# Kernel optimization log

Hardware: AMD Instinct MI355X
Metric: run time of the kernel (lower is better)

Reference implementation:

```python
import jax, jax.numpy as jnp
import numpy as np

LAMBDA = 0.95   # fast-weight decay
ETA = 0.5       # Hebbian write rate
EPS = 1e-5      # LayerNorm epsilon
S_LOOP = 2      # inner read steps


def setup_inputs() -> dict:
    key = jax.random.key(0)
    ks = jax.random.split(key, 3)
    T, B, d_g, d_h = 32, 32, 256, 512
    z_seq = jax.random.normal(ks[0], (T, B, d_g), dtype=jnp.float32)
    # kaiming-uniform-ish / xavier-ish scaled weights
    W_h = jax.random.normal(ks[1], (d_h, d_h), dtype=jnp.float32) * (2.0 / d_h) ** 0.5
    W_g = jax.random.normal(ks[2], (d_h, d_g), dtype=jnp.float32) * (2.0 / (d_h + d_g)) ** 0.5
    b_h = jnp.zeros((d_h,), jnp.float32)
    ln_gamma = jnp.ones((d_h,), jnp.float32)
    ln_beta = jnp.zeros((d_h,), jnp.float32)
    return {"z_seq": z_seq, "W_h": W_h, "W_g": W_g, "b_h": b_h,
            "ln_gamma": ln_gamma, "ln_beta": ln_beta}


def reference(z_seq, W_h, W_g, b_h, ln_gamma, ln_beta):
    T, B, _ = z_seq.shape
    d_h = W_h.shape[0]

    def ln(x):
        mu = jnp.mean(x, axis=-1, keepdims=True)
        var = jnp.mean((x - mu) ** 2, axis=-1, keepdims=True)
        return (x - mu) * jax.lax.rsqrt(var + EPS) * ln_gamma + ln_beta

    def inner_read(h_base, A):
        # h = relu(LN(h_base)); then S fast-weight reads h <- relu(LN(h_base + A h))
        h = jax.nn.relu(ln(h_base))
        for _ in range(S_LOOP):
            Ah = jnp.einsum('bij,bj->bi', A, h)  # [B, d_h]
            h = jax.nn.relu(ln(h_base + Ah))
        return h

    def step(carry, z_t):
        h, A = carry
        h_base = h @ W_h.T + z_t @ W_g.T + b_h  # [B, d_h]
        h = inner_read(h_base, A)
        # Hebbian outer-product write: A <- lambda*A + eta * h h^T
        A = LAMBDA * A + ETA * jnp.einsum('bi,bj->bij', h, h)
        return (h, A), None

    h0 = jnp.zeros((B, d_h), z_seq.dtype)
    A0 = jnp.zeros((B, d_h, d_h), z_seq.dtype)
    (h, A), _ = jax.lax.scan(step, (h0, A0), z_seq[:-1])

    # last step: read-only (no A update)
    h_base = h @ W_h.T + z_seq[-1] @ W_g.T + b_h
    h = inner_read(h_base, A)
    return h
```

## Files before the change

### kernel.cpp

```cpp
#include <hip/hip_runtime.h>

constexpr int T_STEPS = 32;
constexpr int BATCH   = 32;
constexpr int DG      = 256;
constexpr int DH      = 512;
constexpr int NHIST   = 31;
constexpr float LAMBDA_ = 0.95f;
constexpr float ETA_    = 0.5f;
constexpr float EPS_    = 1e-5f;

__global__ __launch_bounds__(512) void aux_kernel(
    const float* __restrict__ z, const float* __restrict__ Wg,
    const float* __restrict__ bh, float* __restrict__ ZG,
    const float* __restrict__ Wh, uint4* __restrict__ Wp) {
  const int tid = threadIdx.x;
  if (blockIdx.x < 256) {
    const int lane = tid & 63;
    const int wave = tid >> 6;
    const int tb0  = blockIdx.x * 4;
    float4 zv[4];
#pragma unroll
    for (int p = 0; p < 4; ++p)
      zv[p] = *reinterpret_cast<const float4*>(z + (size_t)(tb0 + p) * DG + lane * 4);
    for (int k = 0; k < 64; ++k) {
      const int r = wave * 64 + k;
      const float4 wv = *reinterpret_cast<const float4*>(Wg + (size_t)r * DG + lane * 4);
      float a0 = zv[0].x*wv.x + zv[0].y*wv.y + zv[0].z*wv.z + zv[0].w*wv.w;
      float a1 = zv[1].x*wv.x + zv[1].y*wv.y + zv[1].z*wv.z + zv[1].w*wv.w;
      float a2 = zv[2].x*wv.x + zv[2].y*wv.y + zv[2].z*wv.z + zv[2].w*wv.w;
      float a3 = zv[3].x*wv.x + zv[3].y*wv.y + zv[3].z*wv.z + zv[3].w*wv.w;
#pragma unroll
      for (int off = 32; off; off >>= 1) {
        a0 += __shfl_xor(a0, off, 64);
        a1 += __shfl_xor(a1, off, 64);
        a2 += __shfl_xor(a2, off, 64);
        a3 += __shfl_xor(a3, off, 64);
      }
      if (lane == 0) {
        const float bb = bh[r];
        ZG[(size_t)(tb0 + 0) * DH + r] = a0 + bb;
        ZG[(size_t)(tb0 + 1) * DH + r] = a1 + bb;
        ZG[(size_t)(tb0 + 2) * DH + r] = a2 + bb;
        ZG[(size_t)(tb0 + 3) * DH + r] = a3 + bb;
      }
    }
  } else {
    const int v = (blockIdx.x - 256) * 512 + tid;
    const int r = v >> 6;
    const int k8h = v & 63;
    const float4 a = *reinterpret_cast<const float4*>(Wh + (size_t)r * DH + k8h * 8);
    const float4 b = *reinterpret_cast<const float4*>(Wh + (size_t)r * DH + k8h * 8 + 4);
    auto cvt = [](float f) -> uint {
      uint u = __float_as_uint(f);
      return (u + 0x7FFFu + ((u >> 16) & 1u)) >> 16;
    };
    uint4 o;
    o.x = cvt(a.x) | (cvt(a.y) << 16);
    o.y = cvt(a.z) | (cvt(a.w) << 16);
    o.z = cvt(b.x) | (cvt(b.y) << 16);
    o.w = cvt(b.z) | (cvt(b.w) << 16);
    Wp[(size_t)k8h * DH + r] = o;
  }
}

__global__ __launch_bounds__(1024) void rnn_kernel(
    const uint4* __restrict__ Wp, const float* __restrict__ ZG,
    const float* __restrict__ g, const float* __restrict__ be,
    float* __restrict__ out) {
  __shared__ alignas(16) float hist[40][DH];
  __shared__ alignas(16) float4 h4_s[DH / 4];
  __shared__ float part[DH];
  __shared__ float cc[NHIST];
  __shared__ float red1[16], red2[16];
  __shared__ float lam_pow[NHIST];

  float* h_s = reinterpret_cast<float*>(h4_s);
  const int tid  = threadIdx.x;
  const int lane = tid & 63;
  const int wave = tid >> 6;
  const int r    = tid & 511;
  const int kh   = tid >> 9;
  const int b    = blockIdx.x;
  const bool own = (kh == 0);

  if (tid == 0) {
    float p = 1.f;
    for (int k = 0; k < NHIST; ++k) { lam_pow[k] = p; p *= LAMBDA_; }
  }
  float g_r = 0.f, be_r = 0.f;
  if (own) { g_r = g[r]; be_r = be[r]; }

  auto ln = [&](float x) -> float {
    float s1 = own ? x : 0.f;
    float s2 = own ? x * x : 0.f;
#pragma unroll
    for (int off = 32; off; off >>= 1) {
      s1 += __shfl_xor(s1, off, 64);
      s2 += __shfl_xor(s2, off, 64);
    }
    if (lane == 0) { red1[wave] = s1; red2[wave] = s2; }
    __syncthreads();
    float a = 0.f, q = 0.f;
#pragma unroll
    for (int w2 = 0; w2 < 16; ++w2) { a += red1[w2]; q += red2[w2]; }
    const float mu = a * (1.f / DH);
    const float rs = rsqrtf(q * (1.f / DH) - mu * mu + EPS_);
    float hv = 0.f;
    if (own) {
      hv = fmaxf((x - mu) * rs * g_r + be_r, 0.f);
      h_s[r] = hv;
    }
    __syncthreads();
    return hv;
  };

  float hv = 0.f;
  for (int t = 0; t < T_STEPS; ++t) {
    const float* zg = ZG + ((size_t)t * BATCH + b) * DH;
    float xb;

    if (t == 0) {
      xb = own ? zg[r] : 0.f;
    } else {
      const uint4* wp = Wp + (size_t)(kh * 32) * DH + r;
      const float4* hh = h4_s + kh * 64;
      float acc = 0.f;
#pragma unroll 4
      for (int k8 = 0; k8 < 32; ++k8) {
        const uint4 wv = wp[(size_t)k8 * DH];
        const float4 ha = hh[k8 * 2];
        const float4 hb = hh[k8 * 2 + 1];
        acc = fmaf(__uint_as_float(wv.x << 16),           ha.x, acc);
        acc = fmaf(__uint_as_float(wv.x & 0xFFFF0000u),   ha.y, acc);
        acc = fmaf(__uint_as_float(wv.y << 16),           ha.z, acc);
        acc = fmaf(__uint_as_float(wv.y & 0xFFFF0000u),   ha.w, acc);
        acc = fmaf(__uint_as_float(wv.z << 16),           hb.x, acc);
        acc = fmaf(__uint_as_float(wv.z & 0xFFFF0000u),   hb.y, acc);
        acc = fmaf(__uint_as_float(wv.w << 16),           hb.z, acc);
        acc = fmaf(__uint_as_float(wv.w & 0xFFFF0000u),   hb.w, acc);
      }
      if (!own) part[r] = acc;
      __syncthreads();
      xb = own ? (acc + part[r] + zg[r]) : 0.f;
    }

    hv = ln(xb);

    if (t > 0) {
      for (int s = 0; s < 2; ++s) {
        const float4 c0 = *reinterpret_cast<const float4*>(h_s + lane * 8);
        const float4 c1 = *reinterpret_cast<const float4*>(h_s + lane * 8 + 4);
        for (int sp = wave; sp < t; sp += 16) {
          const float* hr = hist[sp];
          const float4 a0 = *reinterpret_cast<const float4*>(hr + lane * 8);
          const float4 a1 = *reinterpret_cast<const float4*>(hr + lane * 8 + 4);
          float d = c0.x*a0.x + c0.y*a0.y + c0.z*a0.z + c0.w*a0.w
                  + c1.x*a1.x + c1.y*a1.y + c1.z*a1.z + c1.w*a1.w;
#pragma unroll
          for (int off = 32; off; off >>= 1) d += __shfl_xor(d, off, 64);
          if (lane == 0) cc[sp] = ETA_ * lam_pow[t - 1 - sp] * d;
        }
        __syncthreads();
        float x2 = xb;
        if (own) {
          float ah = 0.f;
          for (int sp = 0; sp < t; ++sp) ah = fmaf(cc[sp], hist[sp][r], ah);
          x2 = xb + ah;
        }
        hv = ln(x2);
      }
    }

    if (own && t < T_STEPS - 1) hist[t][r] = hv;
  }

  if (own) out[(size_t)b * DH + r] = hv;
}

extern "C" void kernel_launch(void* const* d_in, const int* in_sizes, int n_in,
                              void* d_out, int out_size, void* d_ws, size_t ws_size,
                              hipStream_t stream) {
  const float* z     = (const float*)d_in[0];
  const float* W_h   = (const float*)d_in[1];
  const float* W_g   = (const float*)d_in[2];
  const float* b_h   = (const float*)d_in[3];
  const float* gamma = (const float*)d_in[4];
  const float* beta  = (const float*)d_in[5];
  float* out = (float*)d_out;

  float* ZG = (float*)d_ws;
  uint4* Wp = (uint4*)((char*)d_ws + (size_t)T_STEPS * BATCH * DH * 4);

  aux_kernel<<<dim3(320), dim3(512), 0, stream>>>(z, W_g, b_h, ZG, W_h, Wp);
  rnn_kernel<<<dim3(BATCH), dim3(1024), 0, stream>>>(Wp, ZG, gamma, beta, out);
}
```

Baseline: 340.4 us.

## Use bf16 MFMA for recurrent matvec and pack two batch rows per block

Rewrites the per-step W_h·h product as 16x16x32 bf16 MFMA tiles, with W_h pre-packed into an MFMA-friendly tile layout and h stored as bf16 in shared memory. Each block now processes two batch rows, which halves the grid to 16 blocks and puts all 1024 threads to use instead of half of them being idle during LayerNorm. Half of each wave's weight fragments are prefetched into registers across time steps. The cost is that h is now rounded to bf16 before the matvec, only 2 of 16 MFMA columns do useful work, and fewer CUs are busy.

```diff
diff --git a/kernel.cpp b/kernel.cpp
--- a/kernel.cpp
+++ b/kernel.cpp
@@ -1,13 +1,22 @@
 #include <hip/hip_runtime.h>
+
+typedef __attribute__((ext_vector_type(8))) short short8;
+typedef __attribute__((ext_vector_type(4))) float f32x4;
 
 constexpr int T_STEPS = 32;
 constexpr int BATCH   = 32;
 constexpr int DG      = 256;
 constexpr int DH      = 512;
 constexpr int NHIST   = 31;
+constexpr int WPB     = 2;
 constexpr float LAMBDA_ = 0.95f;
 constexpr float ETA_    = 0.5f;
 constexpr float EPS_    = 1e-5f;
+
+__device__ __forceinline__ uint bf16cvt(float f) {
+  uint u = __float_as_uint(f);
+  return (u + 0x7FFFu + ((u >> 16) & 1u)) >> 16;
+}
 
 __global__ __launch_bounds__(512) void aux_kernel(
     const float* __restrict__ z, const float* __restrict__ Wg,
@@ -45,21 +54,20 @@
       }
     }
   } else {
-    const int v = (blockIdx.x - 256) * 512 + tid;
-    const int r = v >> 6;
-    const int k8h = v & 63;
-    const float4 a = *reinterpret_cast<const float4*>(Wh + (size_t)r * DH + k8h * 8);
-    const float4 b = *reinterpret_cast<const float4*>(Wh + (size_t)r * DH + k8h * 8 + 4);
-    auto cvt = [](float f) -> uint {
-      uint u = __float_as_uint(f);
-      return (u + 0x7FFFu + ((u >> 16) & 1u)) >> 16;
-    };
+    const int f  = (blockIdx.x - 256) * 512 + tid;
+    const int lf = f & 63;
+    const int kk = (f >> 6) & 15;
+    const int mt = f >> 10;
+    const int r  = mt * 16 + (lf & 15);
+    const int k0 = kk * 32 + (lf >> 4) * 8;
+    const float4 a = *reinterpret_cast<const float4*>(Wh + (size_t)r * DH + k0);
+    const float4 b = *reinterpret_cast<const float4*>(Wh + (size_t)r * DH + k0 + 4);
     uint4 o;
-    o.x = cvt(a.x) | (cvt(a.y) << 16);
-    o.y = cvt(a.z) | (cvt(a.w) << 16);
-    o.z = cvt(b.x) | (cvt(b.y) << 16);
-    o.w = cvt(b.z) | (cvt(b.w) << 16);
-    Wp[(size_t)k8h * DH + r] = o;
+    o.x = bf16cvt(a.x) | (bf16cvt(a.y) << 16);
+    o.y = bf16cvt(a.z) | (bf16cvt(a.w) << 16);
+    o.z = bf16cvt(b.x) | (bf16cvt(b.y) << 16);
+    o.w = bf16cvt(b.z) | (bf16cvt(b.w) << 16);
+    Wp[f] = o;
   }
 }
 
@@ -67,32 +75,43 @@
     const uint4* __restrict__ Wp, const float* __restrict__ ZG,
     const float* __restrict__ g, const float* __restrict__ be,
     float* __restrict__ out) {
-  __shared__ alignas(16) float hist[40][DH];
-  __shared__ alignas(16) float4 h4_s[DH / 4];
-  __shared__ float part[DH];
-  __shared__ float cc[NHIST];
-  __shared__ float red1[16], red2[16];
-  __shared__ float lam_pow[NHIST];
-
-  float* h_s = reinterpret_cast<float*>(h4_s);
+  __shared__ float  hist[WPB][NHIST][DH];
+  __shared__ float  part[WPB][DH];
+  __shared__ ushort hbf[WPB][DH];
+  __shared__ float  h_s[WPB][DH];
+  __shared__ float  red1[16], red2[16];
+  __shared__ float  cc[WPB][NHIST + 1];
+  __shared__ float  lam_pow[NHIST];
+
   const int tid  = threadIdx.x;
   const int lane = tid & 63;
   const int wave = tid >> 6;
+  const int bl   = tid >> 9;
   const int r    = tid & 511;
-  const int kh   = tid >> 9;
-  const int b    = blockIdx.x;
-  const bool own = (kh == 0);
+  const int blw  = wave >> 3;
+  const int c    = lane & 15;
+  const int gq   = lane >> 4;
+  const int bg   = blockIdx.x * WPB;
+
+  const int mt0 = 2 * wave, mt1 = 2 * wave + 1;
+  const uint4* wpA0 = Wp + (size_t)mt0 * 1024 + lane;
+  const uint4* wpA1 = Wp + (size_t)mt1 * 1024 + lane;
 
   if (tid == 0) {
     float p = 1.f;
     for (int k = 0; k < NHIST; ++k) { lam_pow[k] = p; p *= LAMBDA_; }
   }
-  float g_r = 0.f, be_r = 0.f;
-  if (own) { g_r = g[r]; be_r = be[r]; }
+  const float g_r = g[r], be_r = be[r];
+
+  uint4 pf0[8], pf1[8];
+#pragma unroll
+  for (int kk = 0; kk < 8; ++kk) {
+    pf0[kk] = wpA0[(size_t)kk * 64];
+    pf1[kk] = wpA1[(size_t)kk * 64];
+  }
 
   auto ln = [&](float x) -> float {
-    float s1 = own ? x : 0.f;
-    float s2 = own ? x * x : 0.f;
+    float s1 = x, s2 = x * x;
 #pragma unroll
     for (int off = 32; off; off >>= 1) {
       s1 += __shfl_xor(s1, off, 64);
@@ -102,79 +121,80 @@
     __syncthreads();
     float a = 0.f, q = 0.f;
 #pragma unroll
-    for (int w2 = 0; w2 < 16; ++w2) { a += red1[w2]; q += red2[w2]; }
+    for (int w2 = 0; w2 < 8; ++w2) { a += red1[bl * 8 + w2]; q += red2[bl * 8 + w2]; }
     const float mu = a * (1.f / DH);
     const float rs = rsqrtf(q * (1.f / DH) - mu * mu + EPS_);
-    float hv = 0.f;
-    if (own) {
-      hv = fmaxf((x - mu) * rs * g_r + be_r, 0.f);
-      h_s[r] = hv;
-    }
+    const float hv = fmaxf((x - mu) * rs * g_r + be_r, 0.f);
+    h_s[bl][r] = hv;
+    hbf[bl][r] = (ushort)bf16cvt(hv);
     __syncthreads();
     return hv;
   };
 
   float hv = 0.f;
   for (int t = 0; t < T_STEPS; ++t) {
-    const float* zg = ZG + ((size_t)t * BATCH + b) * DH;
+    const float zgv = ZG[((size_t)t * BATCH + bg + bl) * DH + r];
     float xb;
 
     if (t == 0) {
-      xb = own ? zg[r] : 0.f;
+      xb = zgv;
     } else {
-      const uint4* wp = Wp + (size_t)(kh * 32) * DH + r;
-      const float4* hh = h4_s + kh * 64;
-      float acc = 0.f;
-#pragma unroll 4
-      for (int k8 = 0; k8 < 32; ++k8) {
-        const uint4 wv = wp[(size_t)k8 * DH];
-        const float4 ha = hh[k8 * 2];
-        const float4 hb = hh[k8 * 2 + 1];
-        acc = fmaf(__uint_as_float(wv.x << 16),           ha.x, acc);
-        acc = fmaf(__uint_as_float(wv.x & 0xFFFF0000u),   ha.y, acc);
-        acc = fmaf(__uint_as_float(wv.y << 16),           ha.z, acc);
-        acc = fmaf(__uint_as_float(wv.y & 0xFFFF0000u),   ha.w, acc);
-        acc = fmaf(__uint_as_float(wv.z << 16),           hb.x, acc);
-        acc = fmaf(__uint_as_float(wv.z & 0xFFFF0000u),   hb.y, acc);
-        acc = fmaf(__uint_as_float(wv.w << 16),           hb.z, acc);
-        acc = fmaf(__uint_as_float(wv.w & 0xFFFF0000u),   hb.w, acc);
-      }
-      if (!own) part[r] = acc;
+      f32x4 acc0 = {0.f, 0.f, 0.f, 0.f}, acc1 = {0.f, 0.f, 0.f, 0.f};
+#pragma unroll
+      for (int kk = 0; kk < 16; ++kk) {
+        const uint4 a0u = (kk < 8) ? pf0[kk] : wpA0[(size_t)kk * 64];
+        const uint4 a1u = (kk < 8) ? pf1[kk] : wpA1[(size_t)kk * 64];
+        uint4 bvu = {0u, 0u, 0u, 0u};
+        if (c < WPB)
+          bvu = *reinterpret_cast<const uint4*>(&hbf[c][kk * 32 + gq * 8]);
+        const short8 a0 = __builtin_bit_cast(short8, a0u);
+        const short8 a1 = __builtin_bit_cast(short8, a1u);
+        const short8 bv = __builtin_bit_cast(short8, bvu);
+        acc0 = __builtin_amdgcn_mfma_f32_16x16x32_bf16(a0, bv, acc0, 0, 0, 0);
+        acc1 = __builtin_amdgcn_mfma_f32_16x16x32_bf16(a1, bv, acc1, 0, 0, 0);
+      }
+      if (t < T_STEPS - 1) {
+#pragma unroll
+        for (int kk = 0; kk < 8; ++kk) {
+          pf0[kk] = wpA0[(size_t)kk * 64];
+          pf1[kk] = wpA1[(size_t)kk * 64];
+        }
+      }
+      if (c < WPB) {
+        *reinterpret_cast<f32x4*>(&part[c][mt0 * 16 + gq * 4]) = acc0;
+        *reinterpret_cast<f32x4*>(&part[c][mt1 * 16 + gq * 4]) = acc1;
+      }
       __syncthreads();
-      xb = own ? (acc + part[r] + zg[r]) : 0.f;
+      xb = part[bl][r] + zgv;
     }
 
     hv = ln(xb);
 
     if (t > 0) {
       for (int s = 0; s < 2; ++s) {
-        const float4 c0 = *reinterpret_cast<const float4*>(h_s + lane * 8);
-        const float4 c1 = *reinterpret_cast<const float4*>(h_s + lane * 8 + 4);
-        for (int sp = wave; sp < t; sp += 16) {
-          const float* hr = hist[sp];
+        const float4 c0 = *reinterpret_cast<const float4*>(&h_s[blw][lane * 8]);
+        const float4 c1 = *reinterpret_cast<const float4*>(&h_s[blw][lane * 8 + 4]);
+        for (int sp = wave & 7; sp < t; sp += 8) {
+          const float* hr = hist[blw][sp];
           const float4 a0 = *reinterpret_cast<const float4*>(hr + lane * 8);
           const float4 a1 = *reinterpret_cast<const float4*>(hr + lane * 8 + 4);
           float d = c0.x*a0.x + c0.y*a0.y + c0.z*a0.z + c0.w*a0.w
                   + c1.x*a1.x + c1.y*a1.y + c1.z*a1.z + c1.w*a1.w;
 #pragma unroll
           for (int off = 32; off; off >>= 1) d += __shfl_xor(d, off, 64);
-          if (lane == 0) cc[sp] = ETA_ * lam_pow[t - 1 - sp] * d;
+          if (lane == 0) cc[blw][sp] = ETA_ * lam_pow[t - 1 - sp] * d;
         }
         __syncthreads();
-        float x2 = xb;
-        if (own) {
-          float ah = 0.f;
-          for (int sp = 0; sp < t; ++sp) ah = fmaf(cc[sp], hist[sp][r], ah);
-          x2 = xb + ah;
-        }
-        hv = ln(x2);
-      }
-    }
-
-    if (own && t < T_STEPS - 1) hist[t][r] = hv;
-  }
-
-  if (own) out[(size_t)b * DH + r] = hv;
+        float ah = 0.f;
+        for (int sp = 0; sp < t; ++sp) ah = fmaf(cc[bl][sp], hist[bl][sp][r], ah);
+        hv = ln(xb + ah);
+      }
+    }
+
+    if (t < T_STEPS - 1) hist[bl][t][r] = hv;
+  }
+
+  out[(size_t)(bg + bl) * DH + r] = hv;
 }
 
 extern "C" void kernel_launch(void* const* d_in, const int* in_sizes, int n_in,
@@ -192,5 +212,5 @@
   uint4* Wp = (uint4*)((char*)d_ws + (size_t)T_STEPS * BATCH * DH * 4);
 
   aux_kernel<<<dim3(320), dim3(512), 0, stream>>>(z, W_g, b_h, ZG, W_h, Wp);
-  rnn_kernel<<<dim3(BATCH), dim3(1024), 0, stream>>>(Wp, ZG, gamma, beta, out);
-}
+  rnn_kernel<<<dim3(BATCH / WPB), dim3(1024), 0, stream>>>(Wp, ZG, gamma, beta, out);
+}
```

Result: slower. 521.9 us (+53.3%).
